# Performance work log

Hardware: AMD Instinct MI355X
Metric: run time of the kernel (lower is better)

The kernel has to match this reference:

```python
import jax, jax.numpy as jnp
import numpy as np

N = 50000
E = 800000
D_IN, D_HID, D_OUT = 256, 256, 128


def _xavier(key, shape):
    fan_in, fan_out = shape
    limit = float(np.sqrt(6.0 / (fan_in + fan_out)))
    return jax.random.uniform(key, shape, jnp.float32, -limit, limit)


def setup_inputs() -> dict:
    key = jax.random.key(0)
    ks = jax.random.split(key, 12)
    x = jax.random.normal(ks[0], (N, D_IN), jnp.float32)
    edge_index = jax.random.randint(ks[1], (2, E), 0, N, dtype=jnp.int64)
    batch = jnp.zeros((N,), jnp.int64)
    # per-layer: message weight W, linear weight LW (stored [in, out]), bias b
    w1 = _xavier(ks[2], (D_IN, D_HID))
    lw1 = _xavier(ks[3], (D_IN, D_HID))
    lb1 = jnp.zeros((D_HID,), jnp.float32)
    w2 = _xavier(ks[4], (D_HID, D_HID))
    lw2 = _xavier(ks[5], (D_HID, D_HID))
    lb2 = jnp.zeros((D_HID,), jnp.float32)
    w3 = _xavier(ks[6], (D_HID, D_OUT))
    lw3 = _xavier(ks[7], (D_HID, D_OUT))
    lb3 = jnp.zeros((D_OUT,), jnp.float32)
    return {"x": x, "edge_index": edge_index, "batch": batch,
            "w1": w1, "lw1": lw1, "lb1": lb1,
            "w2": w2, "lw2": lw2, "lb2": lb2,
            "w3": w3, "lw3": lw3, "lb3": lb3}


def _gcn_layer(x, W, LW, b, row, col, norm):
    # message: norm * (x_j @ W); equivalent and cheaper: transform nodes once, gather
    xw = x @ W                                   # [N, out]
    msg = norm[:, None] * xw[row]                # [E, out]
    agg = jax.ops.segment_sum(msg, col, num_segments=x.shape[0])  # scatter-add at col
    return agg + x @ LW + b                      # residual linear path


def reference(x, edge_index, batch, w1, lw1, lb1, w2, lw2, lb2, w3, lw3, lb3):
    row, col = edge_index[0], edge_index[1]
    ones = jnp.ones((row.shape[0],), x.dtype)
    out_deg = jax.ops.segment_sum(ones, row, num_segments=N)
    in_deg = jax.ops.segment_sum(ones, col, num_segments=N)
    # inf at zero-degree nodes never gets gathered (those nodes have no edges)
    norm = out_deg[row] ** -0.5 * in_deg[col] ** -0.5  # [E]

    h = jax.nn.relu(_gcn_layer(x, w1, lw1, lb1, row, col, norm))
    h = jax.nn.relu(_gcn_layer(h, w2, lw2, lb2, row, col, norm))
    h = jax.nn.sigmoid(_gcn_layer(h, w3, lw3, lb3, row, col, norm))
    return h
```

## Files before the change

### kernel.cpp

```cpp
#include <hip/hip_runtime.h>
#include <hip/hip_bf16.h>
#include <math.h>

#define NNODES 50000
#define NEDGES 800000
#define HNB 128
#define HBINS 50176
#define SCAN_NB 196

typedef short s8v __attribute__((ext_vector_type(8)));
typedef float f4v __attribute__((ext_vector_type(4)));
using bf16 = __hip_bfloat16;

static __device__ __forceinline__ float bflo(unsigned int x) {
    union { unsigned int i; float f; } c; c.i = x << 16; return c.f;
}
static __device__ __forceinline__ float bfhi(unsigned int x) {
    union { unsigned int i; float f; } c; c.i = x & 0xffff0000u; return c.f;
}

static __device__ __forceinline__ void gload16(const void* g, void* l) {
    __builtin_amdgcn_global_load_lds(
        (const __attribute__((address_space(1))) unsigned int*)g,
        (__attribute__((address_space(3))) unsigned int*)l, 16, 0, 0);
}


__global__ void k_packbt(const float* __restrict__ W, const float* __restrict__ LW,
                         bf16* __restrict__ out, int K, int C) {
    int i = blockIdx.x * blockDim.x + threadIdx.x;
    int C2 = 2 * C;
    if (i >= K * C2) return;
    int n = i / K, k = i % K;
    float v = (n < C) ? W[k * C + n] : LW[k * C + (n - C)];
    out[i] = __float2bfloat16(v);
}


__global__ __launch_bounds__(256) void k_hist(const int* __restrict__ ei, ushort* __restrict__ partials) {
    __shared__ unsigned int h32[HBINS / 2];
    int b = blockIdx.x, row = blockIdx.y, t = threadIdx.x;
    for (int i = t; i < HBINS / 2; i += 256) h32[i] = 0;
    __syncthreads();
    const int chunk = NEDGES / HNB;
    int beg = b * chunk, end = beg + chunk;
    const int* p = ei + (size_t)row * NEDGES;
    for (int e = beg + t; e < end; e += 256) {
        int id = p[e];
        atomicAdd(&h32[id >> 1], 1u << (16 * (id & 1)));
    }
    __syncthreads();
    unsigned int* o32 = (unsigned int*)(partials + ((size_t)row * HNB + b) * HBINS);
    for (int i = t; i < HBINS / 2; i += 256) o32[i] = h32[i];
}

__global__ __launch_bounds__(256) void k_hist_reduce(const ushort* __restrict__ partials,
                                                     float* __restrict__ rsqrt_out,
                                                     int* __restrict__ in_cnt,
                                                     int* __restrict__ block_sums) {
    __shared__ int sm[256];
    int row = blockIdx.y;
    int i = blockIdx.x * 256 + threadIdx.x;
    const ushort* p = partials + (size_t)row * HNB * HBINS + i;
    int s = 0;
#pragma unroll 4
    for (int b = 0; b < HNB; ++b) s += p[(size_t)b * HBINS];
    if (row == 0) {
        if (i < NNODES) rsqrt_out[i] = rsqrtf((float)s);
    } else {
        if (i < NNODES) in_cnt[i] = s;
        sm[threadIdx.x] = s;
        __syncthreads();
        for (int off = 128; off > 0; off >>= 1) {
            if (threadIdx.x < off) sm[threadIdx.x] += sm[threadIdx.x + off];
            __syncthreads();
        }
        if (threadIdx.x == 0) block_sums[blockIdx.x] = sm[0];
    }
}


__global__ void k_scan_blocks(const int* __restrict__ block_sums, int* __restrict__ block_base, int nb) {
    __shared__ int s[256];
    int t = threadIdx.x;
    int v = (t < nb) ? block_sums[t] : 0;
    s[t] = v;
    __syncthreads();
    for (int off = 1; off < 256; off <<= 1) {
        int u = (t >= off) ? s[t - off] : 0;
        __syncthreads();
        s[t] += u;
        __syncthreads();
    }
    block_base[t] = s[t] - v;
}

__global__ void k_scan_final(const int* __restrict__ in_cnt, const int* __restrict__ block_base,
                             int* __restrict__ offsets, int* __restrict__ cursor) {
    __shared__ int s[256];
    int b = blockIdx.x, t = threadIdx.x;
    int i = b * 256 + t;
    int v = (i < NNODES) ? in_cnt[i] : 0;
    s[t] = v;
    __syncthreads();
    for (int off = 1; off < 256; off <<= 1) {
        int u = (t >= off) ? s[t - off] : 0;
        __syncthreads();
        s[t] += u;
        __syncthreads();
    }
    int excl = s[t] - v + block_base[b];
    if (i < NNODES) { offsets[i] = excl; cursor[i] = excl; }
    if (i == NNODES - 1) offsets[NNODES] = excl + v;
}

__global__ void k_scatter(const int* __restrict__ ei, int* __restrict__ cursor,
                          int* __restrict__ src_sorted) {
    int e = blockIdx.x * blockDim.x + threadIdx.x;
    if (e < NEDGES) {
        int r = ei[e], c = ei[NEDGES + e];
        int p = atomicAdd(&cursor[c], 1);
        src_sorted[p] = r;
    }
}

template<int D, int C2, int ACT>
__global__ __launch_bounds__(64) void k_agg_fused(const bf16* __restrict__ xwcat,
                                                  const int* __restrict__ offsets,
                                                  const int* __restrict__ src_sorted,
                                                  const float* __restrict__ rsqrt_out,
                                                  const float* __restrict__ bias,
                                                  void* __restrict__ out) {
    const int L = D / 8;
    const int G = 64 / L;
    const int U = 4;
    int lane = threadIdx.x;
    int v = blockIdx.x;
    int g = lane / L, sl = lane % L;

    int beg = offsets[v], end = offsets[v + 1];
    int deg = end - beg;
    int dcap = min(deg, 64);

    int id = 0; float wl = 0.f;
    if (lane < dcap) {
        id = src_sorted[beg + lane];
        wl = rsqrt_out[id];
    }

    float acc[U][8];
#pragma unroll
    for (int u = 0; u < U; ++u)
#pragma unroll
        for (int c = 0; c < 8; ++c) acc[u][c] = 0.f;

    const ushort* base = (const ushort*)xwcat + sl * 8;

    for (int e0 = 0; e0 < dcap; e0 += G * U) {
#pragma unroll
        for (int u = 0; u < U; ++u) {
            int e = e0 + u * G + g;
            int s = __shfl(id, e & 63, 64);
            float w = __shfl(wl, e & 63, 64);
            if (e >= dcap) w = 0.f;
            uint4 q = *(const uint4*)(base + (size_t)s * C2);
            acc[u][0] += w * bflo(q.x); acc[u][1] += w * bfhi(q.x);
            acc[u][2] += w * bflo(q.y); acc[u][3] += w * bfhi(q.y);
            acc[u][4] += w * bflo(q.z); acc[u][5] += w * bfhi(q.z);
            acc[u][6] += w * bflo(q.w); acc[u][7] += w * bfhi(q.w);
        }
    }
    for (int j = beg + 64 + g; j < end; j += G) {
        int s = src_sorted[j];
        float w = rsqrt_out[s];
        uint4 q = *(const uint4*)(base + (size_t)s * C2);
        acc[0][0] += w * bflo(q.x); acc[0][1] += w * bfhi(q.x);
        acc[0][2] += w * bflo(q.y); acc[0][3] += w * bfhi(q.y);
        acc[0][4] += w * bflo(q.z); acc[0][5] += w * bfhi(q.z);
        acc[0][6] += w * bflo(q.w); acc[0][7] += w * bfhi(q.w);
    }

#pragma unroll
    for (int c = 0; c < 8; ++c) acc[0][c] = (acc[0][c] + acc[1][c]) + (acc[2][c] + acc[3][c]);
#pragma unroll
    for (int d = 32; d >= L; d >>= 1) {
#pragma unroll
        for (int c = 0; c < 8; ++c) acc[0][c] += __shfl_down(acc[0][c], d, 64);
    }

    if (lane < L) {
        float sc = (deg > 0) ? rsqrtf((float)deg) : 0.f;
        const ushort* lwp = (const ushort*)xwcat + (size_t)v * C2 + D + sl * 8;
        uint4 ql = *(const uint4*)lwp;
        const float* bp = bias + sl * 8;
        float4 b0 = *(const float4*)bp, b1 = *(const float4*)(bp + 4);
        float h[8];
        h[0] = acc[0][0] * sc + bflo(ql.x) + b0.x;
        h[1] = acc[0][1] * sc + bfhi(ql.x) + b0.y;
        h[2] = acc[0][2] * sc + bflo(ql.y) + b0.z;
        h[3] = acc[0][3] * sc + bfhi(ql.y) + b0.w;
        h[4] = acc[0][4] * sc + bflo(ql.z) + b1.x;
        h[5] = acc[0][5] * sc + bfhi(ql.z) + b1.y;
        h[6] = acc[0][6] * sc + bflo(ql.w) + b1.z;
        h[7] = acc[0][7] * sc + bfhi(ql.w) + b1.w;
        if (ACT == 1) {
            union { bf16 hh[8]; uint4 u; } o;
#pragma unroll
            for (int c = 0; c < 8; ++c) o.hh[c] = __float2bfloat16(fmaxf(h[c], 0.f));
            *(uint4*)((ushort*)out + (size_t)v * D + sl * 8) = o.u;
        } else {
            float r[8];
#pragma unroll
            for (int c = 0; c < 8; ++c) r[c] = 1.f / (1.f + expf(-h[c]));
            float* op = (float*)out + (size_t)v * D + sl * 8;
            *(float4*)op = (float4){r[0], r[1], r[2], r[3]};
            *(float4*)(op + 4) = (float4){r[4], r[5], r[6], r[7]};
        }
    }
}

template<int C2, bool A_BF16>
__global__ __launch_bounds__(256) void k_gemm2(const void* __restrict__ Aptr,
                                               const bf16* __restrict__ BT,
                                               bf16* __restrict__ Out) {
    constexpr int R = NNODES;
    constexpr int GX = (NNODES + 127) / 128;
    constexpr int GY = C2 / 128;
    constexpr int NWG = GX * GY;
    __shared__ bf16 As[128 * 32];
    __shared__ bf16 Bs[128 * 32];

    int o = blockIdx.x;
    constexpr int qq = NWG / 8, rr = NWG % 8;
    int xcd = o & 7, idx = o >> 3;
    int lt = (xcd < rr ? xcd * (qq + 1) : rr * (qq + 1) + (xcd - rr) * qq) + idx;
    int r0 = (lt / GY) * 128;
    int n0 = (lt % GY) * 128;

    int t = threadIdx.x;
    int wave = t >> 6, lane = t & 63;
    int wr = wave >> 1, wc = wave & 1;

    f4v acc[4][4];
#pragma unroll
    for (int mi = 0; mi < 4; ++mi)
#pragma unroll
        for (int ni = 0; ni < 4; ++ni) acc[mi][ni] = (f4v){0.f, 0.f, 0.f, 0.f};

    int sr = t >> 2;
    int sk = (t & 3) * 8;
    int fr = t >> 1, fs = (t & 1) * 16;

    for (int k0 = 0; k0 < 256; k0 += 32) {
        if (A_BF16) {
            const bf16* Ab = (const bf16*)Aptr;
            gload16(Ab + (size_t)min(r0 + sr, R - 1) * 256 + k0 + sk,
                    (char*)As + wave * 1024);
            gload16(Ab + (size_t)min(r0 + sr + 64, R - 1) * 256 + k0 + sk,
                    (char*)As + 4096 + wave * 1024);
        } else {
            const float* Af = (const float*)Aptr + (size_t)min(r0 + fr, R - 1) * 256 + k0 + fs;
            float4 f0 = ((const float4*)Af)[0];
            float4 f1 = ((const float4*)Af)[1];
            float4 f2 = ((const float4*)Af)[2];
            float4 f3 = ((const float4*)Af)[3];
            union { bf16 h[16]; uint4 u[2]; } cv;
            cv.h[0]  = __float2bfloat16(f0.x); cv.h[1]  = __float2bfloat16(f0.y);
            cv.h[2]  = __float2bfloat16(f0.z); cv.h[3]  = __float2bfloat16(f0.w);
            cv.h[4]  = __float2bfloat16(f1.x); cv.h[5]  = __float2bfloat16(f1.y);
            cv.h[6]  = __float2bfloat16(f1.z); cv.h[7]  = __float2bfloat16(f1.w);
            cv.h[8]  = __float2bfloat16(f2.x); cv.h[9]  = __float2bfloat16(f2.y);
            cv.h[10] = __float2bfloat16(f2.z); cv.h[11] = __float2bfloat16(f2.w);
            cv.h[12] = __float2bfloat16(f3.x); cv.h[13] = __float2bfloat16(f3.y);
            cv.h[14] = __float2bfloat16(f3.z); cv.h[15] = __float2bfloat16(f3.w);
            *(uint4*)&As[fr * 32 + fs]     = cv.u[0];
            *(uint4*)&As[fr * 32 + fs + 8] = cv.u[1];
        }
        gload16(BT + (size_t)(n0 + sr) * 256 + k0 + sk,
                (char*)Bs + wave * 1024);
        gload16(BT + (size_t)(n0 + sr + 64) * 256 + k0 + sk,
                (char*)Bs + 4096 + wave * 1024);
        __syncthreads();

        int lr = lane & 15, lk = (lane >> 4) * 8;
        s8v a[4], b[4];
#pragma unroll
        for (int mi = 0; mi < 4; ++mi)
            a[mi] = *(const s8v*)&As[(wr * 64 + mi * 16 + lr) * 32 + lk];
#pragma unroll
        for (int ni = 0; ni < 4; ++ni)
            b[ni] = *(const s8v*)&Bs[(wc * 64 + ni * 16 + lr) * 32 + lk];
#pragma unroll
        for (int mi = 0; mi < 4; ++mi)
#pragma unroll
            for (int ni = 0; ni < 4; ++ni)
                acc[mi][ni] = __builtin_amdgcn_mfma_f32_16x16x32_bf16(a[mi], b[ni], acc[mi][ni], 0, 0, 0);
        __syncthreads();
    }

    int lr = lane & 15, lq = (lane >> 4) * 4;
#pragma unroll
    for (int mi = 0; mi < 4; ++mi) {
#pragma unroll
        for (int rj = 0; rj < 4; ++rj) {
            int grow = r0 + wr * 64 + mi * 16 + lq + rj;
            if (grow < R) {
#pragma unroll
                for (int ni = 0; ni < 4; ++ni) {
                    Out[(size_t)grow * C2 + n0 + wc * 64 + ni * 16 + lr] =
                        __float2bfloat16(acc[mi][ni][rj]);
                }
            }
        }
    }
}


extern "C" void kernel_launch(void* const* d_in, const int* in_sizes, int n_in,
                              void* d_out, int out_size, void* d_ws, size_t ws_size,
                              hipStream_t stream) {
    const float* x   = (const float*)d_in[0];
    const int*   ei  = (const int*)d_in[1];
    const float* w1  = (const float*)d_in[3];
    const float* lw1 = (const float*)d_in[4];
    const float* lb1 = (const float*)d_in[5];
    const float* w2  = (const float*)d_in[6];
    const float* lw2 = (const float*)d_in[7];
    const float* lb2 = (const float*)d_in[8];
    const float* w3  = (const float*)d_in[9];
    const float* lw3 = (const float*)d_in[10];
    const float* lb3 = (const float*)d_in[11];
    float* out = (float*)d_out;

    char* ws = (char*)d_ws;
    size_t off = 0;
    auto alloc = [&](size_t bytes) -> void* {
        void* p = ws + off;
        off += (bytes + 255) & ~(size_t)255;
        return p;
    };
    int*    in_cnt     = (int*)alloc((size_t)HBINS * 4);
    float*  rsqrt_out  = (float*)alloc((size_t)HBINS * 4);
    int*    offsets    = (int*)alloc((size_t)(NNODES + 1) * 4);
    int*    cursor     = (int*)alloc((size_t)NNODES * 4);
    int*    block_sums = (int*)alloc((size_t)256 * 4);
    int*    block_base = (int*)alloc((size_t)256 * 4);
    ushort* partials   = (ushort*)alloc((size_t)2 * HNB * HBINS * 2);
    int*    src_sorted = (int*)alloc((size_t)NEDGES * 4);
    bf16*   wcat1      = (bf16*)alloc((size_t)256 * 512 * 2);
    bf16*   wcat2      = (bf16*)alloc((size_t)256 * 512 * 2);
    bf16*   wcat3      = (bf16*)alloc((size_t)256 * 256 * 2);
    bf16*   xwcat      = (bf16*)alloc((size_t)NNODES * 512 * 2);
    bf16*   h1         = (bf16*)alloc((size_t)NNODES * 256 * 2);
    bf16*   h2         = (bf16*)alloc((size_t)NNODES * 256 * 2);

    k_packbt<<<512, 256, 0, stream>>>(w1, lw1, wcat1, 256, 256);
    k_packbt<<<512, 256, 0, stream>>>(w2, lw2, wcat2, 256, 256);
    k_packbt<<<256, 256, 0, stream>>>(w3, lw3, wcat3, 256, 128);

    k_hist<<<dim3(HNB, 2), 256, 0, stream>>>(ei, partials);
    k_hist_reduce<<<dim3(SCAN_NB, 2), 256, 0, stream>>>(partials, rsqrt_out, in_cnt, block_sums);
    k_scan_blocks<<<1, 256, 0, stream>>>(block_sums, block_base, SCAN_NB);
    k_scan_final<<<SCAN_NB, 256, 0, stream>>>(in_cnt, block_base, offsets, cursor);
    int eblocks = (NEDGES + 255) / 256;
    k_scatter<<<eblocks, 256, 0, stream>>>(ei, cursor, src_sorted);

    k_gemm2<512, false><<<391 * 4, 256, 0, stream>>>(x, wcat1, xwcat);
    k_agg_fused<256, 512, 1><<<NNODES, 64, 0, stream>>>(xwcat, offsets, src_sorted, rsqrt_out, lb1, h1);
    k_gemm2<512, true><<<391 * 4, 256, 0, stream>>>(h1, wcat2, xwcat);
    k_agg_fused<256, 512, 1><<<NNODES, 64, 0, stream>>>(xwcat, offsets, src_sorted, rsqrt_out, lb2, h2);
    k_gemm2<256, true><<<391 * 2, 256, 0, stream>>>(h2, wcat3, xwcat);
    k_agg_fused<128, 256, 2><<<NNODES, 64, 0, stream>>>(xwcat, offsets, src_sorted, rsqrt_out, lb3, out);
}
```

Baseline: 430.3 us.

## Merge weight packing, use global atomic histograms, pack four nodes per agg block

Replaces the three weight-packing launches with one kernel that also zeroes the degree counters. The per-block LDS histograms plus partial-reduction pass become direct global atomic counting followed by a lighter finalize kernel. The aggregation kernels now run four 64-lane node groups per 256-thread block instead of one wave per block. Together these aim to cut launch count, partial-buffer traffic and per-block scheduling overhead, at the cost of global atomic contention in the histogram.

```diff
diff --git a/kernel.cpp b/kernel.cpp
--- a/kernel.cpp
+++ b/kernel.cpp
@@ -4,7 +4,6 @@
 
 #define NNODES 50000
 #define NEDGES 800000
-#define HNB 128
 #define HBINS 50176
 #define SCAN_NB 196
 
@@ -26,57 +25,55 @@
 }
 
 
-__global__ void k_packbt(const float* __restrict__ W, const float* __restrict__ LW,
-                         bf16* __restrict__ out, int K, int C) {
-    int i = blockIdx.x * blockDim.x + threadIdx.x;
-    int C2 = 2 * C;
-    if (i >= K * C2) return;
-    int n = i / K, k = i % K;
+#define M1 (256 * 512)
+#define M2 (256 * 512)
+#define M3 (256 * 256)
+
+__global__ __launch_bounds__(256) void k_packall(
+        const float* __restrict__ w1, const float* __restrict__ lw1,
+        const float* __restrict__ w2, const float* __restrict__ lw2,
+        const float* __restrict__ w3, const float* __restrict__ lw3,
+        bf16* __restrict__ o1, bf16* __restrict__ o2, bf16* __restrict__ o3,
+        int* __restrict__ odeg, int* __restrict__ icnt) {
+    int i = blockIdx.x * 256 + threadIdx.x;
+    if (i < HBINS) odeg[i] = 0;
+    else if (i < 2 * HBINS) icnt[i - HBINS] = 0;
+
+    const float* W; const float* LW; bf16* O; int C; int j;
+    if (i < M1)            { W = w1; LW = lw1; O = o1; C = 256; j = i; }
+    else if (i < M1 + M2)  { W = w2; LW = lw2; O = o2; C = 256; j = i - M1; }
+    else                   { W = w3; LW = lw3; O = o3; C = 128; j = i - M1 - M2; }
+    int n = j >> 8, k = j & 255;
     float v = (n < C) ? W[k * C + n] : LW[k * C + (n - C)];
-    out[i] = __float2bfloat16(v);
-}
-
-
-__global__ __launch_bounds__(256) void k_hist(const int* __restrict__ ei, ushort* __restrict__ partials) {
-    __shared__ unsigned int h32[HBINS / 2];
-    int b = blockIdx.x, row = blockIdx.y, t = threadIdx.x;
-    for (int i = t; i < HBINS / 2; i += 256) h32[i] = 0;
+    O[j] = __float2bfloat16(v);
+}
+
+
+__global__ __launch_bounds__(256) void k_hist_atomic(const int* __restrict__ ei,
+                                                     int* __restrict__ odeg,
+                                                     int* __restrict__ icnt) {
+    int e = blockIdx.x * 256 + threadIdx.x;
+    if (e < NEDGES) {
+        atomicAdd(&odeg[ei[e]], 1);
+        atomicAdd(&icnt[ei[NEDGES + e]], 1);
+    }
+}
+
+__global__ __launch_bounds__(256) void k_finalize(const int* __restrict__ odeg,
+                                                  const int* __restrict__ icnt,
+                                                  float* __restrict__ rsqrt_out,
+                                                  int* __restrict__ block_sums) {
+    __shared__ int sm[256];
+    int i = blockIdx.x * 256 + threadIdx.x;
+    if (i < NNODES) rsqrt_out[i] = rsqrtf((float)odeg[i]);
+    int s = (i < NNODES) ? icnt[i] : 0;
+    sm[threadIdx.x] = s;
     __syncthreads();
-    const int chunk = NEDGES / HNB;
-    int beg = b * chunk, end = beg + chunk;
-    const int* p = ei + (size_t)row * NEDGES;
-    for (int e = beg + t; e < end; e += 256) {
-        int id = p[e];
-        atomicAdd(&h32[id >> 1], 1u << (16 * (id & 1)));
-    }
-    __syncthreads();
-    unsigned int* o32 = (unsigned int*)(partials + ((size_t)row * HNB + b) * HBINS);
-    for (int i = t; i < HBINS / 2; i += 256) o32[i] = h32[i];
-}
-
-__global__ __launch_bounds__(256) void k_hist_reduce(const ushort* __restrict__ partials,
-                                                     float* __restrict__ rsqrt_out,
-                                                     int* __restrict__ in_cnt,
-                                                     int* __restrict__ block_sums) {
-    __shared__ int sm[256];
-    int row = blockIdx.y;
-    int i = blockIdx.x * 256 + threadIdx.x;
-    const ushort* p = partials + (size_t)row * HNB * HBINS + i;
-    int s = 0;
-#pragma unroll 4
-    for (int b = 0; b < HNB; ++b) s += p[(size_t)b * HBINS];
-    if (row == 0) {
-        if (i < NNODES) rsqrt_out[i] = rsqrtf((float)s);
-    } else {
-        if (i < NNODES) in_cnt[i] = s;
-        sm[threadIdx.x] = s;
-        __syncthreads();
-        for (int off = 128; off > 0; off >>= 1) {
-            if (threadIdx.x < off) sm[threadIdx.x] += sm[threadIdx.x + off];
-            __syncthreads();
-        }
-        if (threadIdx.x == 0) block_sums[blockIdx.x] = sm[0];
-    }
+    for (int off = 128; off > 0; off >>= 1) {
+        if (threadIdx.x < off) sm[threadIdx.x] += sm[threadIdx.x + off];
+        __syncthreads();
+    }
+    if (threadIdx.x == 0) block_sums[blockIdx.x] = sm[0];
 }
 
 
@@ -125,7 +122,7 @@
 }
 
 template<int D, int C2, int ACT>
-__global__ __launch_bounds__(64) void k_agg_fused(const bf16* __restrict__ xwcat,
+__global__ __launch_bounds__(256) void k_agg_fused(const bf16* __restrict__ xwcat,
                                                   const int* __restrict__ offsets,
                                                   const int* __restrict__ src_sorted,
                                                   const float* __restrict__ rsqrt_out,
@@ -134,8 +131,9 @@
     const int L = D / 8;
     const int G = 64 / L;
     const int U = 4;
-    int lane = threadIdx.x;
-    int v = blockIdx.x;
+    int t = threadIdx.x;
+    int lane = t & 63;
+    int v = blockIdx.x * 4 + (t >> 6);
     int g = lane / L, sl = lane % L;
 
     int beg = offsets[v], end = offsets[v + 1];
@@ -339,13 +337,13 @@
         off += (bytes + 255) & ~(size_t)255;
         return p;
     };
-    int*    in_cnt     = (int*)alloc((size_t)HBINS * 4);
+    int*    odeg       = (int*)alloc((size_t)HBINS * 4);
+    int*    icnt       = (int*)alloc((size_t)HBINS * 4);
     float*  rsqrt_out  = (float*)alloc((size_t)HBINS * 4);
     int*    offsets    = (int*)alloc((size_t)(NNODES + 1) * 4);
     int*    cursor     = (int*)alloc((size_t)NNODES * 4);
     int*    block_sums = (int*)alloc((size_t)256 * 4);
     int*    block_base = (int*)alloc((size_t)256 * 4);
-    ushort* partials   = (ushort*)alloc((size_t)2 * HNB * HBINS * 2);
     int*    src_sorted = (int*)alloc((size_t)NEDGES * 4);
     bf16*   wcat1      = (bf16*)alloc((size_t)256 * 512 * 2);
     bf16*   wcat2      = (bf16*)alloc((size_t)256 * 512 * 2);
@@ -354,21 +352,20 @@
     bf16*   h1         = (bf16*)alloc((size_t)NNODES * 256 * 2);
     bf16*   h2         = (bf16*)alloc((size_t)NNODES * 256 * 2);
 
-    k_packbt<<<512, 256, 0, stream>>>(w1, lw1, wcat1, 256, 256);
-    k_packbt<<<512, 256, 0, stream>>>(w2, lw2, wcat2, 256, 256);
-    k_packbt<<<256, 256, 0, stream>>>(w3, lw3, wcat3, 256, 128);
-
-    k_hist<<<dim3(HNB, 2), 256, 0, stream>>>(ei, partials);
-    k_hist_reduce<<<dim3(SCAN_NB, 2), 256, 0, stream>>>(partials, rsqrt_out, in_cnt, block_sums);
+    k_packall<<<(M1 + M2 + M3) / 256, 256, 0, stream>>>(
+        w1, lw1, w2, lw2, w3, lw3, wcat1, wcat2, wcat3, odeg, icnt);
+
+    int eblocks = (NEDGES + 255) / 256;
+    k_hist_atomic<<<eblocks, 256, 0, stream>>>(ei, odeg, icnt);
+    k_finalize<<<SCAN_NB, 256, 0, stream>>>(odeg, icnt, rsqrt_out, block_sums);
     k_scan_blocks<<<1, 256, 0, stream>>>(block_sums, block_base, SCAN_NB);
-    k_scan_final<<<SCAN_NB, 256, 0, stream>>>(in_cnt, block_base, offsets, cursor);
-    int eblocks = (NEDGES + 255) / 256;
+    k_scan_final<<<SCAN_NB, 256, 0, stream>>>(icnt, block_base, offsets, cursor);
     k_scatter<<<eblocks, 256, 0, stream>>>(ei, cursor, src_sorted);
 
     k_gemm2<512, false><<<391 * 4, 256, 0, stream>>>(x, wcat1, xwcat);
-    k_agg_fused<256, 512, 1><<<NNODES, 64, 0, stream>>>(xwcat, offsets, src_sorted, rsqrt_out, lb1, h1);
+    k_agg_fused<256, 512, 1><<<NNODES / 4, 256, 0, stream>>>(xwcat, offsets, src_sorted, rsqrt_out, lb1, h1);
     k_gemm2<512, true><<<391 * 4, 256, 0, stream>>>(h1, wcat2, xwcat);
-    k_agg_fused<256, 512, 1><<<NNODES, 64, 0, stream>>>(xwcat, offsets, src_sorted, rsqrt_out, lb2, h2);
+    k_agg_fused<256, 512, 1><<<NNODES / 4, 256, 0, stream>>>(xwcat, offsets, src_sorted, rsqrt_out, lb2, h2);
     k_gemm2<256, true><<<391 * 2, 256, 0, stream>>>(h2, wcat3, xwcat);
-    k_agg_fused<128, 256, 2><<<NNODES, 64, 0, stream>>>(xwcat, offsets, src_sorted, rsqrt_out, lb3, out);
-}
+    k_agg_fused<128, 256, 2><<<NNODES / 4, 256, 0, stream>>>(xwcat, offsets, src_sorted, rsqrt_out, lb3, out);
+}
```

New measurement: 478.4 us. 1.11x slower.
